# Optimization experiments

Hardware: AMD Instinct MI355X
Metric: run time of the kernel (lower is better)

Reference implementation:

```python
import jax, jax.numpy as jnp
import numpy as np

H = 128          # hidden_size
HEADS = 4
D = H // HEADS   # per-head channels (PyG GAT model: out_channels // heads, concat=True)
LAYERS = 2
NEG_SLOPE = 0.2
B, O, V, E = 1024, 20, 400, 840
N = 1 + O + V    # nodes per graph: head + objectives + values
FMIN = float(np.finfo(np.float32).min)


def _gat_conv(x, src, dst, W, a_src, a_dst, b, M):
    """PyG GATConv (v1): x [M,H], src/dst [Etot] (self loops included)."""
    xh = (x @ W).reshape(M, HEADS, D)                       # [M, heads, D]
    al_s = jnp.sum(xh * a_src, axis=-1)                     # [M, heads]
    al_d = jnp.sum(xh * a_dst, axis=-1)                     # [M, heads]
    e = jax.nn.leaky_relu(al_s[src] + al_d[dst], NEG_SLOPE)  # [Etot, heads]
    emax = jax.ops.segment_max(e, dst, num_segments=M)      # every node has a self loop
    ex = jnp.exp(e - emax[dst])
    denom = jax.ops.segment_sum(ex, dst, num_segments=M)
    alpha = ex / denom[dst]                                 # softmax over incoming edges
    out = jax.ops.segment_sum(alpha[:, :, None] * xh[src], dst, num_segments=M)
    return out.reshape(M, H) + b


def setup_inputs() -> dict:
    key = jax.random.key(0)
    ks = jax.random.split(key, 24)
    f = lambda k, shp, s=0.1: (jax.random.normal(k, shp, dtype=jnp.float32) * s)
    inp = {
        'head_node': jax.random.normal(ks[0], (B, 2), dtype=jnp.float32),
        'objective_nodes': jax.random.normal(ks[1], (B, O, 2), dtype=jnp.float32),
        'value_nodes': jax.random.normal(ks[2], (B, V, 5), dtype=jnp.float32),
        'accept_mask': jax.random.uniform(ks[3], (B, 2), dtype=jnp.float32),
        'edge_indices': jax.random.randint(ks[4], (B, 2, E), 0, N, dtype=jnp.int32),
        # encoders
        'We_head': f(ks[5], (2, H), 1.0), 'be_head': jnp.zeros((H,), jnp.float32),
        'We_obj': f(ks[6], (2, H), 1.0), 'be_obj': jnp.zeros((H,), jnp.float32),
        'We_val': f(ks[7], (5, H), 0.7), 'be_val': jnp.zeros((H,), jnp.float32),
        # GAT layers (stacked over LAYERS)
        'W_gat': f(ks[8], (LAYERS, H, H)),
        'a_src': f(ks[9], (LAYERS, HEADS, D)),
        'a_dst': f(ks[10], (LAYERS, HEADS, D)),
        'b_gat': jnp.zeros((LAYERS, H), jnp.float32),
        # output heads
        'W_acc': f(ks[11], (H, 2), 0.01), 'b_acc': jnp.zeros((2,), jnp.float32),
        'W_off': f(ks[12], (H, 1), 0.01), 'b_off': jnp.zeros((1,), jnp.float32),
        'W_vf': f(ks[13], (H, 1)), 'b_vf': jnp.zeros((1,), jnp.float32),
    }
    return inp


def reference(head_node, objective_nodes, value_nodes, accept_mask,
              We_head, be_head, We_obj, be_obj, We_val, be_val,
              W_gat, a_src, a_dst, b_gat,
              W_acc, b_acc, W_off, b_off, W_vf, b_vf,
              edge_indices):
    M = B * N
    # small linear encoders + ReLU
    h_head = jax.nn.relu(head_node @ We_head + be_head)              # [B,H]
    h_obj = jax.nn.relu(objective_nodes @ We_obj + be_obj)           # [B,O,H]
    h_val = jax.nn.relu(value_nodes @ We_val + be_val)               # [B,V,H]
    x = jnp.concatenate([h_head[:, None, :], h_obj, h_val], axis=1).reshape(M, H)
    # batch graphs: offset per-graph node indices, then add self loops
    off = (jnp.arange(B, dtype=jnp.int32) * N)[:, None]
    src = (edge_indices[:, 0, :] + off).reshape(-1)
    dst = (edge_indices[:, 1, :] + off).reshape(-1)
    loops = jnp.arange(M, dtype=jnp.int32)
    src = jnp.concatenate([src, loops])
    dst = jnp.concatenate([dst, loops])
    # GAT stack: ReLU between layers (BasicGNN act) and module applies ReLU after
    for l in range(LAYERS):
        x = _gat_conv(x, src, dst, W_gat[l], a_src[l], a_dst[l], b_gat[l], M)
        x = jax.nn.relu(x)
    h_out = x.reshape(B, N, H)
    h_head_out = h_out[:, 0, :]                                      # [B,H]
    h_val_out = h_out[:, -V:, :]                                     # [B,V,H]
    # masked accept head, offer head over value nodes, value function
    accept_inf_mask = jnp.maximum(jnp.log(accept_mask), FMIN)
    accept_logits = h_head_out @ W_acc + b_acc + accept_inf_mask     # [B,2]
    offer_logits = (h_val_out @ W_off + b_off)[..., 0]               # [B,V]
    vf = h_head_out @ W_vf + b_vf                                    # [B,1]
    # action_logits = cat(accept, offer); vf appended for a single output
    return jnp.concatenate([accept_logits, offer_logits, vf], axis=-1)
```

## Files before the change

kernel.cpp:

```cpp
#include <hip/hip_runtime.h>
#include <math.h>

#define Bb 1024
#define Oo 20
#define Vv 400
#define Ee 840
#define Nn 421
#define Mm (Bb*Nn)
#define Hh 128
#define XST 136
#define FMINF (-3.402823466e38f)

#define PREP_WCONV 16
#define PREP_CSR   1024
#define PREP_ENC   13472

typedef __attribute__((ext_vector_type(8))) short bf8v;
typedef __attribute__((ext_vector_type(4))) float f4v;

__device__ __forceinline__ float lrelu(float x){ return x > 0.f ? x : 0.2f*x; }
__device__ __forceinline__ float bf2f(unsigned int lo16){
    union { unsigned int u; float f; } v; v.u = lo16 << 16; return v.f;
}
__device__ __forceinline__ float bf2fs(short s){ return bf2f((unsigned short)s); }
__device__ __forceinline__ unsigned short f2bf(float f){
    union { float f; unsigned int u; } v; v.f = f;
    unsigned int u = v.u;
    u += 0x7fffu + ((u >> 16) & 1u);
    return (unsigned short)(u >> 16);
}

__global__ __launch_bounds__(512) void prep(
    const float* __restrict__ Wg, unsigned short* __restrict__ Wt,
    const int* __restrict__ ei, int* __restrict__ row_ptr, int* __restrict__ colb,
    const float* __restrict__ hn, const float* __restrict__ on, const float* __restrict__ vn,
    const float* __restrict__ Wh, const float* __restrict__ bh,
    const float* __restrict__ Wo, const float* __restrict__ bo,
    const float* __restrict__ Wv, const float* __restrict__ bv,
    unsigned short* __restrict__ x)
{
    __shared__ __align__(16) unsigned char pool[7680];

    const int blk = blockIdx.x;
    const int tid = threadIdx.x;

    if (blk < PREP_WCONV){
        int idx = blk*512 + tid;
        int l = idx >> 12;
        int n = (idx >> 5) & 127;
        int k0 = (idx & 31) * 4;
        #pragma unroll
        for (int q = 0; q < 4; q++){
            int k = k0 + q;
            Wt[(size_t)l*16384 + n*128 + k] = f2bf(Wg[(size_t)l*16384 + k*128 + n]);
        }
        return;
    }
    if (blk < PREP_WCONV + PREP_CSR){
        unsigned int* keys = (unsigned int*)pool;
        int*          srcL = (int*)(pool + 4096);
        int b = blk - PREP_WCONV;
        const int* eb = ei + (size_t)b*2*Ee;
        for (int e = tid; e < Ee; e += 512){
            srcL[e] = eb[e];
            keys[e] = ((unsigned int)eb[Ee + e] << 10) | (unsigned int)e;
        }
        if (tid < 1024 - Ee) keys[Ee + tid] = 0xFFFFFFFFu;
        __syncthreads();
        for (int k = 2; k <= 1024; k <<= 1){
            for (int j = k >> 1; j > 0; j >>= 1){
                #pragma unroll
                for (int half = 0; half < 2; half++){
                    int i = half*512 + tid;
                    int l = i ^ j;
                    if (l > i){
                        unsigned int a = keys[i], c = keys[l];
                        bool asc = ((i & k) == 0);
                        if (asc ? (a > c) : (a < c)){ keys[i] = c; keys[l] = a; }
                    }
                    __syncthreads();
                }
            }
        }
        for (int i = tid; i < Ee; i += 512){
            unsigned int ky = keys[i];
            int d = (int)(ky >> 10), e = (int)(ky & 1023u);
            colb[b*Ee + i] = srcL[e] | (d << 16);
        }
        if (tid <= Nn){
            unsigned int target = (unsigned int)tid << 10;
            int lo = 0, hi = 1024;
            while (lo < hi){
                int mid = (lo + hi) >> 1;
                if (keys[mid] < target) lo = mid + 1; else hi = mid;
            }
            row_ptr[b*(Nn+1) + tid] = (lo > Ee) ? Ee : lo;
        }
        return;
    }
    {
        float* Wsh = (float*)pool;
        if (tid < 256) Wsh[tid] = Wh[tid];
        else           Wsh[tid] = Wo[tid - 256];
        for (int t = tid; t < 640; t += 512) Wsh[512 + t] = Wv[t];
        if (tid < 128){
            Wsh[1152 + tid] = bh[tid];
            Wsh[1280 + tid] = bo[tid];
            Wsh[1408 + tid] = bv[tid];
        }
        __syncthreads();

        int idx = (blk - PREP_WCONV - PREP_CSR)*512 + tid;
        int row = idx >> 4, seg = idx & 15;
        int b = row / Nn;
        int i = row - b*Nn;
        int c = seg*8;
        float acc[8];
        if (i == 0){
            float h0 = hn[b*2], h1 = hn[b*2+1];
            #pragma unroll
            for (int q = 0; q < 8; q++)
                acc[q] = Wsh[1152 + c + q] + h0*Wsh[c + q] + h1*Wsh[128 + c + q];
        } else if (i < 1 + Oo){
            const float* in = on + ((size_t)b*Oo + (i-1))*2;
            float h0 = in[0], h1 = in[1];
            #pragma unroll
            for (int q = 0; q < 8; q++)
                acc[q] = Wsh[1280 + c + q] + h0*Wsh[256 + c + q] + h1*Wsh[384 + c + q];
        } else {
            const float* in = vn + ((size_t)b*Vv + (i-1-Oo))*5;
            float v0 = in[0], v1 = in[1], v2 = in[2], v3 = in[3], v4 = in[4];
            #pragma unroll
            for (int q = 0; q < 8; q++){
                acc[q] = Wsh[1408 + c + q]
                       + v0*Wsh[512 +           c + q] + v1*Wsh[512 + 128 + c + q]
                       + v2*Wsh[512 + 256 + c + q]     + v3*Wsh[512 + 384 + c + q]
                       + v4*Wsh[512 + 512 + c + q];
            }
        }
        uint4 pk;
        pk.x = ((unsigned int)f2bf(fmaxf(acc[1],0.f)) << 16) | f2bf(fmaxf(acc[0],0.f));
        pk.y = ((unsigned int)f2bf(fmaxf(acc[3],0.f)) << 16) | f2bf(fmaxf(acc[2],0.f));
        pk.z = ((unsigned int)f2bf(fmaxf(acc[5],0.f)) << 16) | f2bf(fmaxf(acc[4],0.f));
        pk.w = ((unsigned int)f2bf(fmaxf(acc[7],0.f)) << 16) | f2bf(fmaxf(acc[6],0.f));
        *(uint4*)(x + (size_t)row*Hh + c) = pk;
    }
}

template<bool LAST>
__global__ __launch_bounds__(512,4) void gat_layer(
    const unsigned short* __restrict__ xin,
    unsigned short* __restrict__ xout,
    const unsigned short* __restrict__ Wt,
    const float* __restrict__ asr,
    const float* __restrict__ adt,
    const float* __restrict__ bg,
    const int* __restrict__ row_ptr,
    const int* __restrict__ colb,
    const float* __restrict__ Woff,
    const float* __restrict__ Wacc,
    const float* __restrict__ Wvf,
    float* __restrict__ partOff,
    float* __restrict__ partHead)
{
    __shared__ unsigned short xh_s[Nn*64];
    __shared__ float als_s[Nn*2], ald_s[Nn*2];
    __shared__ float as_s[64], ad_s[64], bias_s[64];
    __shared__ __align__(16) unsigned char UPool[16384];

    float* p_s    = (float*)UPool;
    float* pself  = (float*)(UPool + 6720);
    int*   colb_s = (int*)  (UPool + 10096);
    int*   rp_s   = (int*)  (UPool + 13456);

    const int lb   = ((int)blockIdx.x & 7)*256 + ((int)blockIdx.x >> 3);
    const int b    = lb >> 1;
    const int half = lb & 1;
    const int chb  = half*64;
    const int tid  = threadIdx.x;
    const size_t base = (size_t)b * Nn;
    const int lane = tid & 63, wave = tid >> 6;
    const int l15 = lane & 15, lhi = lane >> 4;

    #define XH_EL(n_, c_)  xh_s[((n_)<<6) | ((c_) ^ (((n_)&7)<<3))]
    #define XH_CH(n_, c8_) (*(const bf8v*)(xh_s + (((n_)<<6) | (((c8_) ^ ((n_)&7))<<3))))
    #define WS_FRAG(n_, k8_) (*(const bf8v*)((const unsigned short*)UPool + (((n_)<<7) | (((k8_) ^ ((n_)&7))<<3))))

    for (int c = tid; c < 1024; c += 512){
        int n = c >> 4, k8 = c & 15;
        unsigned short* dst = (unsigned short*)UPool + ((n<<7) | ((k8 ^ (n&7))<<3));
        *(uint4*)dst = *(const uint4*)(Wt + (size_t)(chb + n)*Hh + k8*8);
    }
    if (tid < 64)        as_s[tid]       = asr[chb + tid];
    else if (tid < 128)  ad_s[tid-64]    = adt[chb + tid-64];
    else if (tid < 192)  bias_s[tid-128] = bg [chb + tid-128];
    __syncthreads();

    {
        int rt = wave;
        bf8v afN[4];
        {
            int mrow = (rt<<4) + l15; if (mrow >= Nn) mrow = Nn - 1;
            const unsigned short* xr = xin + (base + mrow)*Hh + lhi*8;
            #pragma unroll
            for (int kc = 0; kc < 4; kc++) afN[kc] = *(const bf8v*)(xr + kc*32);
        }
        while (rt < 27){
            bf8v af[4];
            #pragma unroll
            for (int kc = 0; kc < 4; kc++) af[kc] = afN[kc];
            int rtN = rt + 8;
            if (rtN < 27){
                int mrow = (rtN<<4) + l15; if (mrow >= Nn) mrow = Nn - 1;
                const unsigned short* xr = xin + (base + mrow)*Hh + lhi*8;
                #pragma unroll
                for (int kc = 0; kc < 4; kc++) afN[kc] = *(const bf8v*)(xr + kc*32);
            }
            const int row0 = rt << 4;
            #pragma unroll
            for (int ns = 0; ns < 4; ns++){
                const int nn = ns*16 + l15;
                f4v acc = {0.f,0.f,0.f,0.f};
                #pragma unroll
                for (int kc = 0; kc < 4; kc++)
                    acc = __builtin_amdgcn_mfma_f32_16x16x32_bf16(af[kc], WS_FRAG(nn, kc*4 + lhi), acc, 0,0,0);
                #pragma unroll
                for (int r = 0; r < 4; r++){
                    int m = row0 + lhi*4 + r;
                    if (m < Nn) XH_EL(m, nn) = f2bf(acc[r]);
                }
            }
            rt = rtN;
        }
    }
    __syncthreads();

    for (int idx = tid; idx < Nn*2; idx += 512){
        int n = idx >> 1, h2 = idx & 1;
        float s = 0.f, d = 0.f;
        #pragma unroll
        for (int j = 0; j < 4; j++){
            bf8v xv = XH_CH(n, h2*4 + j);
            #pragma unroll
            for (int q = 0; q < 8; q++){
                float xf = bf2fs(xv[q]);
                s += xf * as_s[h2*32 + j*8 + q];
                d += xf * ad_s[h2*32 + j*8 + q];
            }
        }
        als_s[idx] = s; ald_s[idx] = d;
    }
    for (int e = tid; e < Ee; e += 512) colb_s[e] = colb[b*Ee + e];
    for (int i2 = tid; i2 <= Nn; i2 += 512) rp_s[i2] = row_ptr[b*(Nn+1) + i2];
    __syncthreads();

    for (int idx = tid; idx < Ee*2; idx += 512){
        int e = idx >> 1, h2 = idx & 1;
        int pk = colb_s[e];
        int s = pk & 0xffff, dd = pk >> 16;
        p_s[idx] = __expf(fminf(lrelu(als_s[s*2 + h2] + ald_s[dd*2 + h2]), 60.f));
    }
    for (int idx = tid; idx < Nn*2; idx += 512)
        pself[idx] = __expf(fminf(lrelu(als_s[idx] + ald_s[idx]), 60.f));
    __syncthreads();

    {
        const int grp = tid >> 2, lane4 = tid & 3;
        const int c80 = lane4*2;
        const int ch0 = lane4*16;
        const int h2  = lane4 >> 1;
        float wof[16];
        if (LAST){
            #pragma unroll
            for (int q = 0; q < 16; q++) wof[q] = Woff[chb + ch0 + q];
        }
        for (int n = grp; n < Nn; n += 128){
            float den = pself[n*2 + h2];
            float a[16];
            {
                bf8v xv0 = XH_CH(n, c80);
                bf8v xv1 = XH_CH(n, c80 + 1);
                #pragma unroll
                for (int q = 0; q < 8; q++){
                    a[q]     = den * bf2fs(xv0[q]);
                    a[8 + q] = den * bf2fs(xv1[q]);
                }
            }
            int rp0 = rp_s[n], rp1 = rp_s[n+1];
            for (int e = rp0; e < rp1; e++){
                int s = colb_s[e] & 0xffff;
                float p = p_s[e*2 + h2];
                bf8v sv0 = XH_CH(s, c80);
                bf8v sv1 = XH_CH(s, c80 + 1);
                den += p;
                #pragma unroll
                for (int q = 0; q < 8; q++){
                    a[q]     += p * bf2fs(sv0[q]);
                    a[8 + q] += p * bf2fs(sv1[q]);
                }
            }
            float inv = 1.f/den;
            float o[16];
            #pragma unroll
            for (int q = 0; q < 16; q++) o[q] = fmaxf(a[q]*inv + bias_s[ch0 + q], 0.f);
            if (!LAST){
                unsigned int pk[8];
                #pragma unroll
                for (int q2 = 0; q2 < 8; q2++)
                    pk[q2] = ((unsigned int)f2bf(o[q2*2+1]) << 16) | f2bf(o[q2*2]);
                unsigned short* dst = xout + (base + n)*Hh + chb + ch0;
                *(uint4*)dst       = make_uint4(pk[0],pk[1],pk[2],pk[3]);
                *(uint4*)(dst + 8) = make_uint4(pk[4],pk[5],pk[6],pk[7]);
            } else {
                if (n >= 1 + Oo){
                    float po = 0.f;
                    #pragma unroll
                    for (int q = 0; q < 16; q++) po += o[q]*wof[q];
                    po += __shfl_xor(po,1); po += __shfl_xor(po,2);
                    if (lane4 == 0) partOff[((size_t)b*Vv + (n - 1 - Oo))*2 + half] = po;
                } else if (n == 0){
                    float pa0 = 0.f, pa1 = 0.f, pvf = 0.f;
                    #pragma unroll
                    for (int q = 0; q < 16; q++){
                        int gc = chb + ch0 + q;
                        float ov = o[q];
                        pa0 += ov*Wacc[gc*2]; pa1 += ov*Wacc[gc*2+1]; pvf += ov*Wvf[gc];
                    }
                    pa0 += __shfl_xor(pa0,1); pa0 += __shfl_xor(pa0,2);
                    pa1 += __shfl_xor(pa1,1); pa1 += __shfl_xor(pa1,2);
                    pvf += __shfl_xor(pvf,1); pvf += __shfl_xor(pvf,2);
                    if (lane4 == 0){
                        partHead[b*6 + half*3 + 0] = pa0;
                        partHead[b*6 + half*3 + 1] = pa1;
                        partHead[b*6 + half*3 + 2] = pvf;
                    }
                }
            }
        }
    }
    #undef XH_EL
    #undef XH_CH
    #undef WS_FRAG
}

__global__ __launch_bounds__(128) void heads2(const float* __restrict__ partOff,
    const float* __restrict__ partHead, const float* __restrict__ am,
    const float* __restrict__ bacc, const float* __restrict__ boff,
    const float* __restrict__ bvf, float* __restrict__ out)
{
    int b = blockIdx.x, tid = threadIdx.x;
    float bo = boff[0];
    for (int v = tid; v < Vv; v += 128){
        const float* p = partOff + ((size_t)b*Vv + v)*2;
        out[(size_t)b*403 + 2 + v] = p[0] + p[1] + bo;
    }
    if (tid == 0){
        out[(size_t)b*403 + 0]   = partHead[b*6+0] + partHead[b*6+3] + bacc[0] + fmaxf(logf(am[b*2+0]), FMINF);
        out[(size_t)b*403 + 1]   = partHead[b*6+1] + partHead[b*6+4] + bacc[1] + fmaxf(logf(am[b*2+1]), FMINF);
        out[(size_t)b*403 + 402] = partHead[b*6+2] + partHead[b*6+5] + bvf[0];
    }
}

__global__ __launch_bounds__(512) void gat_fused(
    unsigned short* __restrict__ xg,
    const unsigned short* __restrict__ Wt,
    const float* __restrict__ asr, const float* __restrict__ adt,
    const float* __restrict__ bg,
    const int* __restrict__ row_ptr, const int* __restrict__ colb,
    const float* __restrict__ am,
    const float* __restrict__ Wacc, const float* __restrict__ bacc,
    const float* __restrict__ Woff, const float* __restrict__ boff,
    const float* __restrict__ Wvf,  const float* __restrict__ bvf,
    float* __restrict__ out)
{
    __shared__ unsigned short xh_s[Nn][XST];
    __shared__ float als_s[Nn][4];
    __shared__ float ald_s[Nn][4];
    __shared__ float as_s[Hh], ad_s[Hh], bias_s[Hh];
    __shared__ __align__(16) unsigned char UPool[32768];

    float* p_s    = (float*)UPool;
    float* pself  = (float*)(UPool + 13440);
    int*   colb_s = (int*)  (UPool + 20176);
    int*   rp_s   = (int*)  (UPool + 23536);

    const int b   = blockIdx.x;
    const int tid = threadIdx.x;
    const size_t base = (size_t)b * Nn;
    const int lane = tid & 63, wave = tid >> 6;
    const int l15 = lane & 15, lhi = lane >> 4;

    #define BFRAG(n_, kb_) (*(const bf8v*)(UPool + ((n_)<<8) + ((kb_) ^ (((n_)&7)<<4))))

    for (int l = 0; l < 2; l++){
        const unsigned short* Wl = Wt + (size_t)l*16384;
        for (int c = tid; c < 2048; c += 512){
            int n = c >> 4, ck = c & 15;
            int dstb = (n << 8) + ((ck*16) ^ ((n & 7) << 4));
            *(uint4*)(UPool + dstb) = *(const uint4*)(Wl + n*Hh + ck*8);
        }
        if (tid < Hh)        as_s[tid]        = asr[l*Hh + tid];
        else if (tid < 2*Hh) ad_s[tid-Hh]     = adt[l*Hh + tid-Hh];
        else if (tid < 3*Hh) bias_s[tid-2*Hh] = bg [l*Hh + tid-2*Hh];
        __syncthreads();

        {
            int rt = wave;
            bf8v afN[4];
            {
                int mrow = (rt<<4) + l15; if (mrow >= Nn) mrow = Nn - 1;
                const unsigned short* xr = xg + (base + mrow)*Hh + lhi*8;
                #pragma unroll
                for (int kc = 0; kc < 4; kc++) afN[kc] = *(const bf8v*)(xr + kc*32);
            }
            while (rt < 27){
                bf8v af[4];
                #pragma unroll
                for (int kc = 0; kc < 4; kc++) af[kc] = afN[kc];
                int rtN = rt + 8;
                if (rtN < 27){
                    int mrow = (rtN<<4) + l15; if (mrow >= Nn) mrow = Nn - 1;
                    const unsigned short* xr = xg + (base + mrow)*Hh + lhi*8;
                    #pragma unroll
                    for (int kc = 0; kc < 4; kc++) afN[kc] = *(const bf8v*)(xr + kc*32);
                }
                const int row0 = rt << 4;
                #pragma unroll
                for (int ct2 = 0; ct2 < 4; ct2++){
                    const int c0 = ct2*32;
                    const int n0 = c0 + l15, n1 = n0 + 16;
                    f4v acc0 = {0.f,0.f,0.f,0.f}, acc1 = {0.f,0.f,0.f,0.f};
                    #pragma unroll
                    for (int kc = 0; kc < 4; kc++){
                        const int kb = kc*64 + lhi*16;
                        acc0 = __builtin_amdgcn_mfma_f32_16x16x32_bf16(af[kc], BFRAG(n0, kb), acc0, 0,0,0);
                        acc1 = __builtin_amdgcn_mfma_f32_16x16x32_bf16(af[kc], BFRAG(n1, kb), acc1, 0,0,0);
                    }
                    #pragma unroll
                    for (int r = 0; r < 4; r++){
                        int m = row0 + lhi*4 + r;
                        if (m < Nn){
                            xh_s[m][n0] = f2bf(acc0[r]);
                            xh_s[m][n1] = f2bf(acc1[r]);
                        }
                    }
                }
                rt = rtN;
            }
        }
        __syncthreads();

        for (int idx = tid; idx < Nn*4; idx += 512){
            int n = idx >> 2, h = idx & 3;
            const unsigned short* xr = &xh_s[n][h*32];
            float s = 0.f, d = 0.f;
            #pragma unroll
            for (int c4 = 0; c4 < 4; c4++){
                bf8v xv = *(const bf8v*)(xr + c4*8);
                #pragma unroll
                for (int q = 0; q < 8; q++){
                    float xf = bf2fs(xv[q]);
                    s += xf * as_s[h*32 + c4*8 + q];
                    d += xf * ad_s[h*32 + c4*8 + q];
                }
            }
            als_s[n][h] = s; ald_s[n][h] = d;
        }
        for (int e = tid; e < Ee; e += 512) colb_s[e] = colb[b*Ee + e];
        for (int i2 = tid; i2 <= Nn; i2 += 512) rp_s[i2] = row_ptr[b*(Nn+1) + i2];
        __syncthreads();

        for (int idx = tid; idx < Nn*4; idx += 512){
            int n = idx >> 2, h = idx & 3;
            float aldh = ald_s[n][h];
            pself[idx] = __expf(fminf(lrelu(als_s[n][h] + aldh), 60.f));
            int rp0 = rp_s[n], rp1 = rp_s[n+1];
            for (int e = rp0; e < rp1; e++){
                int s = colb_s[e] & 0xffff;
                p_s[e*4 + h] = __expf(fminf(lrelu(als_s[s][h] + aldh), 60.f));
            }
        }
        __syncthreads();

        {
            const int ha  = l15 >> 2;
            const int ch0 = l15 * 8;
            for (int n0 = wave*4; n0 < Nn; n0 += 32){
                int n = n0 + lhi;
                if (n < Nn){
                    float den = pself[n*4 + ha];
                    bf8v xv = *(const bf8v*)&xh_s[n][ch0];
                    float a[8];
                    #pragma unroll
                    for (int q = 0; q < 8; q++) a[q] = den * bf2fs(xv[q]);
                    int rp0 = rp_s[n], rp1 = rp_s[n+1];
                    for (int e = rp0; e < rp1; e++){
                        int s = colb_s[e] & 0xffff;
                        float pC = p_s[e*4 + ha];
                        den += pC;
                        bf8v sv = *(const bf8v*)&xh_s[s][ch0];
                        #pragma unroll
                        for (int q = 0; q < 8; q++) a[q] += pC * bf2fs(sv[q]);
                    }
                    float inv = 1.f/den;
                    unsigned int pk[4];
                    #pragma unroll
                    for (int q2 = 0; q2 < 4; q2++){
                        float o0 = fmaxf(a[q2*2]  *inv + bias_s[ch0 + q2*2],     0.f);
                        float o1 = fmaxf(a[q2*2+1]*inv + bias_s[ch0 + q2*2 + 1], 0.f);
                        pk[q2] = ((unsigned int)f2bf(o1) << 16) | f2bf(o0);
                    }
                    *(uint4*)(xg + (base + n)*Hh + ch0) = make_uint4(pk[0],pk[1],pk[2],pk[3]);
                }
            }
        }
        __syncthreads();
    }

    {
        const int ch0 = l15 * 8;
        for (int v0 = wave*4; v0 < Vv; v0 += 32){
            int v = v0 + lhi;
            if (v < Vv){
                bf8v xv = *(const bf8v*)(xg + (base + 1 + Oo + v)*Hh + ch0);
                float s = 0.f;
                #pragma unroll
                for (int q = 0; q < 8; q++) s += bf2fs(xv[q]) * Woff[ch0 + q];
                s += __shfl_xor(s,1); s += __shfl_xor(s,2);
                s += __shfl_xor(s,4); s += __shfl_xor(s,8);
                if (l15 == 0) out[(size_t)b*403 + 2 + v] = s + boff[0];
            }
        }
        if (wave == 0){
            int k0 = lane*2;
            unsigned int uv = *(const unsigned int*)(xg + base*Hh + k0);
            float x0 = bf2f(uv & 0xffffu), x1 = bf2f(uv >> 16);
            float s0 = x0*Wacc[k0*2]     + x1*Wacc[(k0+1)*2];
            float s1 = x0*Wacc[k0*2 + 1] + x1*Wacc[(k0+1)*2 + 1];
            float s2 = x0*Wvf[k0]        + x1*Wvf[k0+1];
            #pragma unroll
            for (int t = 1; t < 64; t <<= 1){
                s0 += __shfl_xor(s0, t);
                s1 += __shfl_xor(s1, t);
                s2 += __shfl_xor(s2, t);
            }
            if (lane == 0){
                out[(size_t)b*403 + 0]   = s0 + bacc[0] + fmaxf(logf(am[b*2+0]), FMINF);
                out[(size_t)b*403 + 1]   = s1 + bacc[1] + fmaxf(logf(am[b*2+1]), FMINF);
                out[(size_t)b*403 + 402] = s2 + bvf[0];
            }
        }
    }
    #undef BFRAG
}

extern "C" void kernel_launch(void* const* d_in, const int* in_sizes, int n_in,
                              void* d_out, int out_size, void* d_ws, size_t ws_size,
                              hipStream_t stream)
{
    const float* head_node = (const float*)d_in[0];
    const float* obj  = (const float*)d_in[1];
    const float* val  = (const float*)d_in[2];
    const float* am   = (const float*)d_in[3];
    const int*   ei   = (const int*)  d_in[4];
    const float* Weh  = (const float*)d_in[5];
    const float* beh  = (const float*)d_in[6];
    const float* Weo  = (const float*)d_in[7];
    const float* beo  = (const float*)d_in[8];
    const float* Wev  = (const float*)d_in[9];
    const float* bev  = (const float*)d_in[10];
    const float* Wg   = (const float*)d_in[11];
    const float* asr  = (const float*)d_in[12];
    const float* adt  = (const float*)d_in[13];
    const float* bgat = (const float*)d_in[14];
    const float* Wacc = (const float*)d_in[15];
    const float* bacc = (const float*)d_in[16];
    const float* Woff = (const float*)d_in[17];
    const float* boff = (const float*)d_in[18];
    const float* Wvf  = (const float*)d_in[19];
    const float* bvf  = (const float*)d_in[20];

    const size_t xBytes  = (size_t)Mm*Hh*2;
    const size_t rpBytes = (size_t)Bb*(Nn+1)*4;
    const size_t cbBytes = (size_t)Bb*Ee*4;
    const size_t wtBytes = (size_t)2*Hh*Hh*2;
    const size_t poBytes = (size_t)Bb*Vv*2*4;
    const size_t phBytes = (size_t)Bb*6*4;
    const size_t needFast = 2*xBytes + rpBytes + cbBytes + wtBytes + poBytes + phBytes;

    char* ws = (char*)d_ws;
    unsigned short* x0 = (unsigned short*)ws;          ws += xBytes;
    const bool fast = (ws_size >= needFast);
    unsigned short* x1 = fast ? (unsigned short*)ws : x0;
    if (fast) ws += xBytes;
    int* row_ptr = (int*)ws;                           ws += rpBytes;
    int* colb    = (int*)ws;                           ws += cbBytes;
    unsigned short* WtB = (unsigned short*)ws;         ws += wtBytes;
    float* partOff  = (float*)ws;                      ws += poBytes;
    float* partHead = (float*)ws;                      ws += phBytes;

    prep<<<PREP_WCONV + PREP_CSR + PREP_ENC, 512, 0, stream>>>(
        Wg, WtB, ei, row_ptr, colb,
        head_node, obj, val, Weh, beh, Weo, beo, Wev, bev, x0);
    if (fast){
        gat_layer<false><<<2048, 512, 0, stream>>>(x0, x1, WtB, asr, adt, bgat,
                                                   row_ptr, colb, Woff, Wacc, Wvf,
                                                   partOff, partHead);
        gat_layer<true><<<2048, 512, 0, stream>>>(x1, x0, WtB + 16384, asr + Hh, adt + Hh, bgat + Hh,
                                                  row_ptr, colb, Woff, Wacc, Wvf,
                                                  partOff, partHead);
        heads2<<<Bb, 128, 0, stream>>>(partOff, partHead, am, bacc, boff, bvf, (float*)d_out);
    } else {
        gat_fused<<<Bb, 512, 0, stream>>>(x0, WtB, asr, adt, bgat, row_ptr, colb,
                                          am, Wacc, bacc, Woff, boff, Wvf, bvf,
                                          (float*)d_out);
    }
}
```

Baseline: 197.3 us.

## Fuse node encoders into first GAT layer and drop encoded-feature buffer

Moves the per-node input encoders (linear plus ReLU to bf16) out of the prep kernel and computes them directly inside the first GAT layer, feeding the MFMA projection from registers. This removes a full write and read of the encoded node features from global memory and frees one workspace buffer, so layer 1 writes into x0 and layer 2 reads it back. Encoder weights are now rounded to bf16 in shared memory, which changes numerics slightly. Each wave also recomputes the encoder per row tile, and the first layer's shared-memory use grows. The fallback path gains a separate encode kernel.

```diff
diff --git a/kernel.cpp b/kernel.cpp
--- a/kernel.cpp
+++ b/kernel.cpp
@@ -13,7 +13,6 @@
 
 #define PREP_WCONV 16
 #define PREP_CSR   1024
-#define PREP_ENC   13472
 
 typedef __attribute__((ext_vector_type(8))) short bf8v;
 typedef __attribute__((ext_vector_type(4))) float f4v;
@@ -32,12 +31,7 @@
 
 __global__ __launch_bounds__(512) void prep(
     const float* __restrict__ Wg, unsigned short* __restrict__ Wt,
-    const int* __restrict__ ei, int* __restrict__ row_ptr, int* __restrict__ colb,
-    const float* __restrict__ hn, const float* __restrict__ on, const float* __restrict__ vn,
-    const float* __restrict__ Wh, const float* __restrict__ bh,
-    const float* __restrict__ Wo, const float* __restrict__ bo,
-    const float* __restrict__ Wv, const float* __restrict__ bv,
-    unsigned short* __restrict__ x)
+    const int* __restrict__ ei, int* __restrict__ row_ptr, int* __restrict__ colb)
 {
     __shared__ __align__(16) unsigned char pool[7680];
 
@@ -56,7 +50,7 @@
         }
         return;
     }
-    if (blk < PREP_WCONV + PREP_CSR){
+    {
         unsigned int* keys = (unsigned int*)pool;
         int*          srcL = (int*)(pool + 4096);
         int b = blk - PREP_WCONV;
@@ -96,58 +90,65 @@
             }
             row_ptr[b*(Nn+1) + tid] = (lo > Ee) ? Ee : lo;
         }
-        return;
-    }
-    {
-        float* Wsh = (float*)pool;
-        if (tid < 256) Wsh[tid] = Wh[tid];
-        else           Wsh[tid] = Wo[tid - 256];
-        for (int t = tid; t < 640; t += 512) Wsh[512 + t] = Wv[t];
-        if (tid < 128){
-            Wsh[1152 + tid] = bh[tid];
-            Wsh[1280 + tid] = bo[tid];
-            Wsh[1408 + tid] = bv[tid];
-        }
-        __syncthreads();
-
-        int idx = (blk - PREP_WCONV - PREP_CSR)*512 + tid;
-        int row = idx >> 4, seg = idx & 15;
-        int b = row / Nn;
-        int i = row - b*Nn;
-        int c = seg*8;
-        float acc[8];
-        if (i == 0){
-            float h0 = hn[b*2], h1 = hn[b*2+1];
-            #pragma unroll
-            for (int q = 0; q < 8; q++)
-                acc[q] = Wsh[1152 + c + q] + h0*Wsh[c + q] + h1*Wsh[128 + c + q];
-        } else if (i < 1 + Oo){
-            const float* in = on + ((size_t)b*Oo + (i-1))*2;
-            float h0 = in[0], h1 = in[1];
-            #pragma unroll
-            for (int q = 0; q < 8; q++)
-                acc[q] = Wsh[1280 + c + q] + h0*Wsh[256 + c + q] + h1*Wsh[384 + c + q];
-        } else {
-            const float* in = vn + ((size_t)b*Vv + (i-1-Oo))*5;
-            float v0 = in[0], v1 = in[1], v2 = in[2], v3 = in[3], v4 = in[4];
-            #pragma unroll
-            for (int q = 0; q < 8; q++){
-                acc[q] = Wsh[1408 + c + q]
-                       + v0*Wsh[512 +           c + q] + v1*Wsh[512 + 128 + c + q]
-                       + v2*Wsh[512 + 256 + c + q]     + v3*Wsh[512 + 384 + c + q]
-                       + v4*Wsh[512 + 512 + c + q];
-            }
-        }
-        uint4 pk;
-        pk.x = ((unsigned int)f2bf(fmaxf(acc[1],0.f)) << 16) | f2bf(fmaxf(acc[0],0.f));
-        pk.y = ((unsigned int)f2bf(fmaxf(acc[3],0.f)) << 16) | f2bf(fmaxf(acc[2],0.f));
-        pk.z = ((unsigned int)f2bf(fmaxf(acc[5],0.f)) << 16) | f2bf(fmaxf(acc[4],0.f));
-        pk.w = ((unsigned int)f2bf(fmaxf(acc[7],0.f)) << 16) | f2bf(fmaxf(acc[6],0.f));
-        *(uint4*)(x + (size_t)row*Hh + c) = pk;
-    }
-}
-
-template<bool LAST>
+    }
+}
+
+__global__ __launch_bounds__(256) void encode(const float* __restrict__ hn,
+    const float* __restrict__ on, const float* __restrict__ vn,
+    const float* __restrict__ Wh, const float* __restrict__ bh,
+    const float* __restrict__ Wo, const float* __restrict__ bo,
+    const float* __restrict__ Wv, const float* __restrict__ bv,
+    unsigned short* __restrict__ x)
+{
+    __shared__ float Wsh[1536];
+    int tid = threadIdx.x;
+    Wsh[tid]       = Wh[tid];
+    Wsh[256 + tid] = Wo[tid];
+    for (int t = tid; t < 640; t += 256) Wsh[512 + t] = Wv[t];
+    if (tid < 128){
+        Wsh[1152 + tid] = bh[tid];
+        Wsh[1280 + tid] = bo[tid];
+        Wsh[1408 + tid] = bv[tid];
+    }
+    __syncthreads();
+
+    int idx = blockIdx.x*256 + tid;
+    int row = idx >> 4, seg = idx & 15;
+    int b = row / Nn;
+    int i = row - b*Nn;
+    int c = seg*8;
+    float acc[8];
+    if (i == 0){
+        float h0 = hn[b*2], h1 = hn[b*2+1];
+        #pragma unroll
+        for (int q = 0; q < 8; q++)
+            acc[q] = Wsh[1152 + c + q] + h0*Wsh[c + q] + h1*Wsh[128 + c + q];
+    } else if (i < 1 + Oo){
+        const float* in = on + ((size_t)b*Oo + (i-1))*2;
+        float h0 = in[0], h1 = in[1];
+        #pragma unroll
+        for (int q = 0; q < 8; q++)
+            acc[q] = Wsh[1280 + c + q] + h0*Wsh[256 + c + q] + h1*Wsh[384 + c + q];
+    } else {
+        const float* in = vn + ((size_t)b*Vv + (i-1-Oo))*5;
+        float v0 = in[0], v1 = in[1], v2 = in[2], v3 = in[3], v4 = in[4];
+        #pragma unroll
+        for (int q = 0; q < 8; q++){
+            acc[q] = Wsh[1408 + c + q]
+                   + v0*Wsh[512 +           c + q] + v1*Wsh[512 + 128 + c + q]
+                   + v2*Wsh[512 + 256 + c + q]     + v3*Wsh[512 + 384 + c + q]
+                   + v4*Wsh[512 + 512 + c + q];
+        }
+    }
+    uint4 pk;
+    pk.x = ((unsigned int)f2bf(fmaxf(acc[1],0.f)) << 16) | f2bf(fmaxf(acc[0],0.f));
+    pk.y = ((unsigned int)f2bf(fmaxf(acc[3],0.f)) << 16) | f2bf(fmaxf(acc[2],0.f));
+    pk.z = ((unsigned int)f2bf(fmaxf(acc[5],0.f)) << 16) | f2bf(fmaxf(acc[4],0.f));
+    pk.w = ((unsigned int)f2bf(fmaxf(acc[7],0.f)) << 16) | f2bf(fmaxf(acc[6],0.f));
+    *(uint4*)(x + (size_t)row*Hh + c) = pk;
+}
+
+template<bool FIRST, bool LAST>
 __global__ __launch_bounds__(512,4) void gat_layer(
     const unsigned short* __restrict__ xin,
     unsigned short* __restrict__ xout,
@@ -157,6 +158,12 @@
     const float* __restrict__ bg,
     const int* __restrict__ row_ptr,
     const int* __restrict__ colb,
+    const float* __restrict__ hn,
+    const float* __restrict__ on,
+    const float* __restrict__ vn,
+    const float* __restrict__ Weh, const float* __restrict__ beh,
+    const float* __restrict__ Weo, const float* __restrict__ beo,
+    const float* __restrict__ Wev, const float* __restrict__ bev,
     const float* __restrict__ Woff,
     const float* __restrict__ Wacc,
     const float* __restrict__ Wvf,
@@ -166,6 +173,7 @@
     __shared__ unsigned short xh_s[Nn*64];
     __shared__ float als_s[Nn*2], ald_s[Nn*2];
     __shared__ float as_s[64], ad_s[64], bias_s[64];
+    __shared__ unsigned short ew_s[FIRST ? 1536 : 8];
     __shared__ __align__(16) unsigned char UPool[16384];
 
     float* p_s    = (float*)UPool;
@@ -194,9 +202,66 @@
     if (tid < 64)        as_s[tid]       = asr[chb + tid];
     else if (tid < 128)  ad_s[tid-64]    = adt[chb + tid-64];
     else if (tid < 192)  bias_s[tid-128] = bg [chb + tid-128];
+    if (FIRST){
+        for (int t = tid; t < 1536; t += 512){
+            float v;
+            if (t < 256)       v = Weh[t];
+            else if (t < 512)  v = Weo[t-256];
+            else if (t < 1152) v = Wev[t-512];
+            else if (t < 1280) v = beh[t-1152];
+            else if (t < 1408) v = beo[t-1280];
+            else               v = bev[t-1408];
+            ew_s[t] = f2bf(v);
+        }
+    }
     __syncthreads();
 
-    {
+    if (FIRST){
+        for (int rt = wave; rt < 27; rt += 8){
+            int m = (rt<<4) + l15; if (m >= Nn) m = Nn - 1;
+            float f0, f1, f2, f3, f4; int wb, bb;
+            if (m == 0){
+                f0 = hn[b*2]; f1 = hn[b*2+1]; f2 = f3 = f4 = 0.f; wb = 0; bb = 1152;
+            } else if (m < 1 + Oo){
+                const float* in = on + ((size_t)b*Oo + (m-1))*2;
+                f0 = in[0]; f1 = in[1]; f2 = f3 = f4 = 0.f; wb = 256; bb = 1280;
+            } else {
+                const float* in = vn + ((size_t)b*Vv + (m-1-Oo))*5;
+                f0 = in[0]; f1 = in[1]; f2 = in[2]; f3 = in[3]; f4 = in[4]; wb = 512; bb = 1408;
+            }
+            bf8v af[4];
+            #pragma unroll
+            for (int kc = 0; kc < 4; kc++){
+                int c = kc*32 + lhi*8;
+                bf8v wB = *(const bf8v*)(ew_s + bb + c);
+                bf8v w0 = *(const bf8v*)(ew_s + wb + c);
+                bf8v w1 = *(const bf8v*)(ew_s + wb + 128 + c);
+                bf8v w2 = *(const bf8v*)(ew_s + wb + 256 + c);
+                bf8v w3 = *(const bf8v*)(ew_s + wb + 384 + c);
+                bf8v w4 = *(const bf8v*)(ew_s + wb + 512 + c);
+                #pragma unroll
+                for (int i = 0; i < 8; i++){
+                    float acc = bf2fs(wB[i]) + f0*bf2fs(w0[i]) + f1*bf2fs(w1[i])
+                              + f2*bf2fs(w2[i]) + f3*bf2fs(w3[i]) + f4*bf2fs(w4[i]);
+                    af[kc][i] = (short)f2bf(fmaxf(acc, 0.f));
+                }
+            }
+            const int row0 = rt << 4;
+            #pragma unroll
+            for (int ns = 0; ns < 4; ns++){
+                const int nn = ns*16 + l15;
+                f4v acc = {0.f,0.f,0.f,0.f};
+                #pragma unroll
+                for (int kc = 0; kc < 4; kc++)
+                    acc = __builtin_amdgcn_mfma_f32_16x16x32_bf16(af[kc], WS_FRAG(nn, kc*4 + lhi), acc, 0,0,0);
+                #pragma unroll
+                for (int r = 0; r < 4; r++){
+                    int mm = row0 + lhi*4 + r;
+                    if (mm < Nn) XH_EL(mm, nn) = f2bf(acc[r]);
+                }
+            }
+        }
+    } else {
         int rt = wave;
         bf8v afN[4];
         {
@@ -586,31 +651,30 @@
     const size_t wtBytes = (size_t)2*Hh*Hh*2;
     const size_t poBytes = (size_t)Bb*Vv*2*4;
     const size_t phBytes = (size_t)Bb*6*4;
-    const size_t needFast = 2*xBytes + rpBytes + cbBytes + wtBytes + poBytes + phBytes;
+    const size_t needFast = xBytes + rpBytes + cbBytes + wtBytes + poBytes + phBytes;
 
     char* ws = (char*)d_ws;
     unsigned short* x0 = (unsigned short*)ws;          ws += xBytes;
-    const bool fast = (ws_size >= needFast);
-    unsigned short* x1 = fast ? (unsigned short*)ws : x0;
-    if (fast) ws += xBytes;
     int* row_ptr = (int*)ws;                           ws += rpBytes;
     int* colb    = (int*)ws;                           ws += cbBytes;
     unsigned short* WtB = (unsigned short*)ws;         ws += wtBytes;
     float* partOff  = (float*)ws;                      ws += poBytes;
     float* partHead = (float*)ws;                      ws += phBytes;
-
-    prep<<<PREP_WCONV + PREP_CSR + PREP_ENC, 512, 0, stream>>>(
-        Wg, WtB, ei, row_ptr, colb,
-        head_node, obj, val, Weh, beh, Weo, beo, Wev, bev, x0);
+    const bool fast = (ws_size >= needFast);
+
+    prep<<<PREP_WCONV + PREP_CSR, 512, 0, stream>>>(Wg, WtB, ei, row_ptr, colb);
     if (fast){
-        gat_layer<false><<<2048, 512, 0, stream>>>(x0, x1, WtB, asr, adt, bgat,
-                                                   row_ptr, colb, Woff, Wacc, Wvf,
-                                                   partOff, partHead);
-        gat_layer<true><<<2048, 512, 0, stream>>>(x1, x0, WtB + 16384, asr + Hh, adt + Hh, bgat + Hh,
-                                                  row_ptr, colb, Woff, Wacc, Wvf,
-                                                  partOff, partHead);
+        gat_layer<true,false><<<2048, 512, 0, stream>>>(
+            nullptr, x0, WtB, asr, adt, bgat, row_ptr, colb,
+            head_node, obj, val, Weh, beh, Weo, beo, Wev, bev,
+            Woff, Wacc, Wvf, partOff, partHead);
+        gat_layer<false,true><<<2048, 512, 0, stream>>>(
+            x0, nullptr, WtB + 16384, asr + Hh, adt + Hh, bgat + Hh, row_ptr, colb,
+            head_node, obj, val, Weh, beh, Weo, beo, Wev, bev,
+            Woff, Wacc, Wvf, partOff, partHead);
         heads2<<<Bb, 128, 0, stream>>>(partOff, partHead, am, bacc, boff, bvf, (float*)d_out);
     } else {
+        encode<<<Mm*16/256, 256, 0, stream>>>(head_node, obj, val, Weh, beh, Weo, beo, Wev, bev, x0);
         gat_fused<<<Bb, 512, 0, stream>>>(x0, WtB, asr, adt, bgat, row_ptr, colb,
                                           am, Wacc, bacc, Woff, boff, Wvf, bvf,
                                           (float*)d_out);
```

Result: slower. 215.2 us (+9.1%).
